# Kernel tuning notes

Hardware: AMD Instinct MI355X
Metric: run time of the kernel (lower is better)

## Reference

```python
import jax, jax.numpy as jnp
import numpy as np

B, S, C, H, E, K = 8, 512, 768, 12, 8, 2
MLP_H = int(C * 4.0)
HD = C // H
ROUTER_REG = 0.01
LN_EPS = 1e-5


def setup_inputs() -> dict:
    key = jax.random.key(0)
    ks = jax.random.split(key, 8)

    def w(k, shape, fan_in):
        return (jax.random.normal(k, shape, dtype=jnp.float32) / np.sqrt(fan_in)).astype(jnp.float32)

    return {
        "x": jax.random.normal(ks[0], (B, S, C), dtype=jnp.float32),
        "expert_tokens": w(ks[1], (E, C), C),
        "ln1_g": jnp.ones((E, C), jnp.float32),
        "ln1_b": jnp.zeros((E, C), jnp.float32),
        "qkv_w": w(ks[2], (E, C, 3 * C), C),
        "qkv_b": jnp.zeros((E, 3 * C), jnp.float32),
        "proj_w": w(ks[3], (E, C, C), C),
        "proj_b": jnp.zeros((E, C), jnp.float32),
        "ln2_g": jnp.ones((E, C), jnp.float32),
        "ln2_b": jnp.zeros((E, C), jnp.float32),
        "fc1_w": w(ks[4], (E, C, MLP_H), C),
        "fc1_b": jnp.zeros((E, MLP_H), jnp.float32),
        "fc2_w": w(ks[5], (E, MLP_H, C), MLP_H),
        "fc2_b": jnp.zeros((E, C), jnp.float32),
    }


def _layernorm(x, g, b):
    mu = jnp.mean(x, axis=-1, keepdims=True)
    var = jnp.mean(jnp.square(x - mu), axis=-1, keepdims=True)
    return (x - mu) * jax.lax.rsqrt(var + LN_EPS) * g + b


def _block(x, p):
    # One transformer Block (pre-LN attention + MLP), params for a single expert.
    ln1_g, ln1_b, qkv_w, qkv_b, proj_w, proj_b, ln2_g, ln2_b, fc1_w, fc1_b, fc2_w, fc2_b = p
    h = _layernorm(x, ln1_g, ln1_b)
    qkv = (h @ qkv_w + qkv_b).reshape(B, S, 3, H, HD)
    q, k, v = qkv[:, :, 0], qkv[:, :, 1], qkv[:, :, 2]  # [B,S,H,HD]
    # NOTE: original code MULTIPLIES by sqrt(head_dim) (scale = head_dim**0.5).
    scale = jnp.float32(np.sqrt(HD))
    attn = jax.nn.softmax(jnp.einsum('bqhd,bkhd->bhqk', q, k) * scale, axis=-1)
    o = jnp.einsum('bhqk,bkhd->bqhd', attn, v).reshape(B, S, C)
    x = x + (o @ proj_w + proj_b)
    h2 = _layernorm(x, ln2_g, ln2_b)
    x = x + (jax.nn.gelu(h2 @ fc1_w + fc1_b, approximate=False) @ fc2_w + fc2_b)
    return x


def reference(x, expert_tokens, ln1_g, ln1_b, qkv_w, qkv_b, proj_w, proj_b,
              ln2_g, ln2_b, fc1_w, fc1_b, fc2_w, fc2_b):
    # Router
    router_logits = jnp.einsum('bsc,nc->bsn', x, expert_tokens) / jnp.float32(np.sqrt(C))
    router_probs = jax.nn.softmax(router_logits, axis=-1)
    top_k_probs, top_k_idx = jax.lax.top_k(router_probs, K)  # [B,S,K]
    top_k_probs = top_k_probs / jnp.sum(top_k_probs, axis=-1, keepdims=True)

    # Dense all-expert compute (sequential over experts to bound memory)
    params = (ln1_g, ln1_b, qkv_w, qkv_b, proj_w, proj_b, ln2_g, ln2_b,
              fc1_w, fc1_b, fc2_w, fc2_b)
    expert_out = jax.lax.map(lambda p: _block(x, p), params)  # [E,B,S,C]
    expert_out = jnp.transpose(expert_out, (1, 2, 0, 3))       # [B,S,E,C]

    # Top-k gather and weighted combine
    sel = jnp.take_along_axis(expert_out, top_k_idx[..., None], axis=2)  # [B,S,K,C]
    combine = jnp.sum(sel * top_k_probs[..., None], axis=2)
    out = x + combine

    # Load-balance auxiliary loss
    counts = jnp.sum(jax.nn.one_hot(top_k_idx, E, dtype=jnp.float32), axis=(0, 1, 2))
    f_i = counts / jnp.float32(B * S * K)
    P_i = jnp.mean(router_probs, axis=(0, 1))
    balance_loss = E * jnp.sum(f_i * P_i) + ROUTER_REG * jnp.linalg.norm(expert_tokens)
    return out, balance_loss
```

## Files before the change

kernel.cpp:

```cpp
#include <hip/hip_runtime.h>
#include <hip/hip_bf16.h>

#define BB 8
#define SS 512
#define CC 768
#define HH 12
#define HD 64
#define EE 8
#define KK 2
#define MLPH 3072
#define NT (BB*SS)
#define NOUT (NT*CC)

#define SLOTB      68059136ull
#define SLOT_U16   34029568ull
#define SLOT_F32   17014784ull

typedef unsigned int u32;
typedef unsigned short u16;
typedef __attribute__((ext_vector_type(8))) short short8;
typedef __attribute__((ext_vector_type(4))) float f32x4;

__device__ __forceinline__ u16 f2bf(float f) {
    u32 u = __builtin_bit_cast(u32, f);
    u32 r = (u + 0x7fffu + ((u >> 16) & 1u)) >> 16;
    return (u16)r;
}
__device__ __forceinline__ float bf2f(u16 h) {
    u32 u = ((u32)h) << 16;
    return __builtin_bit_cast(float, u);
}
__device__ __forceinline__ void gl_lds16(const void* g, void* l) {
    __builtin_amdgcn_global_load_lds(
        (const __attribute__((address_space(1))) u32*)g,
        (__attribute__((address_space(3))) u32*)l, 16, 0, 0);
}
__device__ __forceinline__ void swz_rc(int bid, int& bm, int& bn) {
    int xcd = bid & 7, off = bid >> 3;
    bm = (xcd * 4 + (off & 3)) * 128;
    bn = (off >> 2) * 128;
}

__device__ __forceinline__ void stg_dp(const u16* __restrict__ A, const u16* __restrict__ B,
                                       int ldk, u16* sA, u16* sB, int t, int tid)
{
    int wid = tid >> 6, lane = tid & 63;
#pragma unroll
    for (int rd = 0; rd < 2; rd++) {
        int cb = rd * 256 + wid * 64;
        int c = cb + lane;
        gl_lds16(A + (size_t)(c >> 2) * ldk + t * 32 + (c & 3) * 8, sA + cb * 8);
    }
#pragma unroll
    for (int rd = 0; rd < 2; rd++) {
        int cb = rd * 256 + wid * 64;
        int c = cb + lane;
        gl_lds16(B + (size_t)(c >> 2) * ldk + t * 32 + (c & 3) * 8, sB + cb * 8);
    }
}

__global__ __launch_bounds__(256) void router_kernel(const float* __restrict__ x,
    const float* __restrict__ et, float* __restrict__ W, float* __restrict__ stats)
{
    __shared__ float etl[EE * CC];
    __shared__ float pred[4][2 * EE];
    int tid = threadIdx.x;
    for (int i = tid; i < EE * CC; i += 256) etl[i] = et[i];
    __syncthreads();
    int wid = tid >> 6, lane = tid & 63;
    float psum[EE] = {}, csum[EE] = {};
    for (int i = 0; i < 2; i++) {
        int t = blockIdx.x * 8 + wid * 2 + i;
        const float* xr = x + (size_t)t * CC;
        float acc[EE] = {};
        for (int c = lane; c < CC; c += 64) {
            float xv = xr[c];
#pragma unroll
            for (int e = 0; e < EE; e++) acc[e] += xv * etl[e * CC + c];
        }
#pragma unroll
        for (int e = 0; e < EE; e++)
            for (int off = 1; off < 64; off <<= 1) acc[e] += __shfl_xor(acc[e], off, 64);
        if (lane == 0) {
            const float inv = 0.03608439182435161f;
            float l[EE], m = -1e30f;
#pragma unroll
            for (int e = 0; e < EE; e++) { l[e] = acc[e] * inv; m = fmaxf(m, l[e]); }
            float p[EE], sum = 0.f;
#pragma unroll
            for (int e = 0; e < EE; e++) { p[e] = __expf(l[e] - m); sum += p[e]; }
            int i1 = 0;
#pragma unroll
            for (int e = 1; e < EE; e++) if (p[e] > p[i1]) i1 = e;
            int i2 = -1;
#pragma unroll
            for (int e = 0; e < EE; e++) if (e != i1 && (i2 < 0 || p[e] > p[i2])) i2 = e;
            float wn = p[i1] + p[i2];
#pragma unroll
            for (int e = 0; e < EE; e++) W[t * EE + e] = 0.f;
            W[t * EE + i1] = p[i1] / wn;
            W[t * EE + i2] = p[i2] / wn;
#pragma unroll
            for (int e = 0; e < EE; e++) psum[e] += p[e] / sum;
            csum[i1] += 1.f; csum[i2] += 1.f;
        }
    }
    if (lane == 0) {
#pragma unroll
        for (int e = 0; e < EE; e++) { pred[wid][e] = psum[e]; pred[wid][EE + e] = csum[e]; }
    }
    __syncthreads();
    if (tid < 2 * EE) {
        float s = pred[0][tid] + pred[1][tid] + pred[2][tid] + pred[3][tid];
        atomicAdd(&stats[tid], s);
    }
}

template<int MODE>
__global__ __launch_bounds__(256) void ln_kernel(const float* __restrict__ x, size_t xslot,
    u16* __restrict__ out_hi, u16* __restrict__ out_lo, size_t oslot)
{
    int t = blockIdx.x;
    int eb = blockIdx.y;
    const float* xr = x + (size_t)eb * xslot + (size_t)t * CC;
    __shared__ float red[256];
    int tid = threadIdx.x;
    float v[3];
    float s = 0.f;
#pragma unroll
    for (int i = 0; i < 3; i++) { v[i] = xr[tid + i * 256]; s += v[i]; }
    red[tid] = s; __syncthreads();
    for (int off = 128; off > 0; off >>= 1) { if (tid < off) red[tid] += red[tid + off]; __syncthreads(); }
    float mu = red[0] / (float)CC;
    __syncthreads();
    float s2 = 0.f;
#pragma unroll
    for (int i = 0; i < 3; i++) { float d = v[i] - mu; s2 += d * d; }
    red[tid] = s2; __syncthreads();
    for (int off = 128; off > 0; off >>= 1) { if (tid < off) red[tid] += red[tid + off]; __syncthreads(); }
    float var = red[0] / (float)CC;
    float sc = rsqrtf(var + 1e-5f);
#pragma unroll
    for (int i = 0; i < 3; i++) {
        int c = tid + i * 256;
        float val = (v[i] - mu) * sc;
        u16 hi = f2bf(val);
        out_hi[(size_t)eb * oslot + (size_t)t * CC + c] = hi;
        if (MODE) out_lo[(size_t)eb * oslot + (size_t)t * CC + c] = f2bf(val - bf2f(hi));
    }
}

__global__ __launch_bounds__(256) void prep_expert(
    const float* __restrict__ qkv_w0, const float* __restrict__ qkv_b0,
    const float* __restrict__ proj_w0,
    const float* __restrict__ fc1_w0, const float* __restrict__ fc1_b0,
    const float* __restrict__ fc2_w0,
    const float* __restrict__ g1_0, const float* __restrict__ b1_0,
    const float* __restrict__ g2_0, const float* __restrict__ b2_0,
    u16* __restrict__ qkvTh, u16* __restrict__ qkvTl,
    u16* __restrict__ projT, u16* __restrict__ fc1T, u16* __restrict__ fc2T,
    float* __restrict__ biasq, float* __restrict__ biasf1, int ebase)
{
    __shared__ float tile[32][33];
    __shared__ float bsh[CC];
    __shared__ float redg[256];
    int bid = blockIdx.x;
    int eb = blockIdx.y;
    int ge = ebase + eb;
    int tid = threadIdx.x;
    const float* qkv_w = qkv_w0 + (size_t)ge * CC * 3 * CC;
    const float* qkv_b = qkv_b0 + (size_t)ge * 3 * CC;
    const float* proj_w = proj_w0 + (size_t)ge * CC * CC;
    const float* fc1_w = fc1_w0 + (size_t)ge * CC * MLPH;
    const float* fc1_b = fc1_b0 + (size_t)ge * MLPH;
    const float* fc2_w = fc2_w0 + (size_t)ge * MLPH * CC;
    const float* g1 = g1_0 + (size_t)ge * CC;
    const float* b1 = b1_0 + (size_t)ge * CC;
    const float* g2 = g2_0 + (size_t)ge * CC;
    const float* b2 = b2_0 + (size_t)ge * CC;

    if (bid < 6912) {
        const float* src; const float* scale = nullptr;
        u16 *dh, *dl = nullptr; int N, Kd, n0, k0;
        if (bid < 1728) {
            src = qkv_w; scale = g1;
            dh = qkvTh + (size_t)eb * SLOT_U16; dl = qkvTl + (size_t)eb * SLOT_U16;
            N = 2304; Kd = 768; n0 = (bid % 72) * 32; k0 = (bid / 72) * 32;
        } else if (bid < 2304) {
            int i = bid - 1728;
            src = proj_w; dh = projT + (size_t)eb * SLOT_U16; N = 768; Kd = 768;
            n0 = (i % 24) * 32; k0 = (i / 24) * 32;
        } else if (bid < 4608) {
            int i = bid - 2304;
            src = fc1_w; scale = g2; dh = fc1T + (size_t)eb * SLOT_U16; N = 3072; Kd = 768;
            n0 = (i % 96) * 32; k0 = (i / 96) * 32;
        } else {
            int i = bid - 4608;
            src = fc2_w; dh = fc2T + (size_t)eb * SLOT_U16; N = 768; Kd = 3072;
            n0 = (i % 24) * 32; k0 = (i / 24) * 32;
        }
        int tx = tid & 31, ty = tid >> 5;
#pragma unroll
        for (int i = 0; i < 32; i += 8) {
            float v = src[(size_t)(k0 + ty + i) * N + n0 + tx];
            if (scale) v *= scale[k0 + ty + i];
            tile[ty + i][tx] = v;
        }
        __syncthreads();
#pragma unroll
        for (int i = 0; i < 32; i += 8) {
            float v = tile[tx][ty + i];
            u16 hi = f2bf(v);
            dh[(size_t)(n0 + ty + i) * Kd + k0 + tx] = hi;
            if (dl) dl[(size_t)(n0 + ty + i) * Kd + k0 + tx] = f2bf(v - bf2f(hi));
        }
    } else {
        const float* bv; const float* wsrc; const float* badd;
        float* dst; int N, n0;
        if (bid < 6984) { bv = b1; wsrc = qkv_w; badd = qkv_b; dst = biasq + (size_t)eb * SLOT_F32; N = 2304; n0 = (bid - 6912) * 32; }
        else            { bv = b2; wsrc = fc1_w; badd = fc1_b; dst = biasf1 + (size_t)eb * SLOT_F32; N = MLPH; n0 = (bid - 6984) * 32; }
        for (int i = tid; i < CC; i += 256) bsh[i] = bv[i];
        __syncthreads();
        int g = tid & 31, l8 = tid >> 5;
        int n = n0 + g;
        float acc = 0.f;
        for (int k = l8; k < CC; k += 8) acc += bsh[k] * wsrc[(size_t)k * N + n];
        redg[tid] = acc; __syncthreads();
        if (tid < 32) {
            float sum = 0.f;
#pragma unroll
            for (int i = 0; i < 8; i++) sum += redg[tid + i * 32];
            dst[n0 + tid] = sum + badd[n0 + tid];
        }
    }
}

__global__ __launch_bounds__(256) void gemm_qkv_dp(
    const u16* __restrict__ Ah, const u16* __restrict__ Al,
    const u16* __restrict__ Bh0, const u16* __restrict__ Bl0,
    const float* __restrict__ biasq0, u16* __restrict__ qk_hi0,
    u16* __restrict__ qk_lo0, u16* __restrict__ vtout0)
{
    __shared__ __align__(16) u16 sBh[3][128 * 32];
    __shared__ __align__(16) u16 sBl[3][128 * 32];
    const int NTILE = CC / 32;
    int tid = threadIdx.x;
    int eb = blockIdx.y;
    int bm, bn;
    swz_rc(blockIdx.x, bm, bn);
    bool qk = (bn < 1536);
    int wid = tid >> 6, lane = tid & 63;
    int wr = wid >> 1, wc = wid & 1;
    int la = lane & 15, lb = lane >> 4;

    const u16* Bh = Bh0 + (size_t)eb * SLOT_U16 + (size_t)bn * CC;
    const u16* Bl = Bl0 + (size_t)eb * SLOT_U16 + (size_t)bn * CC;
    const u16* Ahb = Ah + (size_t)bm * CC;
    const u16* Alb = Al + (size_t)bm * CC;

    auto STG = [&](int s, int t) {
#pragma unroll
        for (int rd = 0; rd < 2; rd++) {
            int cb = rd * 256 + wid * 64;
            int c = cb + lane;
            gl_lds16(Bh + (size_t)(c >> 2) * CC + t * 32 + (c & 3) * 8, &sBh[s][(size_t)cb * 8]);
        }
        if (qk) {
#pragma unroll
            for (int rd = 0; rd < 2; rd++) {
                int cb = rd * 256 + wid * 64;
                int c = cb + lane;
                gl_lds16(Bl + (size_t)(c >> 2) * CC + t * 32 + (c & 3) * 8, &sBl[s][(size_t)cb * 8]);
            }
        }
    };

    f32x4 acc[4][4];
#pragma unroll
    for (int i = 0; i < 4; i++)
#pragma unroll
        for (int j = 0; j < 4; j++) acc[i][j] = (f32x4){0.f, 0.f, 0.f, 0.f};

    STG(0, 0);
    STG(1, 1);

    for (int t = 0; t < NTILE; t++) {
        if (t < NTILE - 1) {
            if (qk) asm volatile("s_waitcnt vmcnt(4)" ::: "memory");
            else    asm volatile("s_waitcnt vmcnt(2)" ::: "memory");
        } else {
            asm volatile("s_waitcnt vmcnt(0)" ::: "memory");
        }
        __builtin_amdgcn_s_barrier();
        asm volatile("" ::: "memory");

        short8 avh[4], avl[4];
#pragma unroll
        for (int i = 0; i < 4; i++)
            avh[i] = *(const short8*)(Ahb + (size_t)(wr * 64 + i * 16 + la) * CC + t * 32 + lb * 8);
        if (qk) {
#pragma unroll
            for (int i = 0; i < 4; i++)
                avl[i] = *(const short8*)(Alb + (size_t)(wr * 64 + i * 16 + la) * CC + t * 32 + lb * 8);
        }

        const u16* cBh = &sBh[t % 3][0];
        const u16* cBl = &sBl[t % 3][0];
        __builtin_amdgcn_s_setprio(1);
#pragma unroll
        for (int j = 0; j < 4; j++) {
            short8 bvh = *(const short8*)(cBh + (size_t)(wc * 64 + j * 16 + la) * 32 + lb * 8);
#pragma unroll
            for (int i = 0; i < 4; i++)
                acc[i][j] = __builtin_amdgcn_mfma_f32_16x16x32_bf16(avh[i], bvh, acc[i][j], 0, 0, 0);
        }
        if (qk) {
#pragma unroll
            for (int j = 0; j < 4; j++) {
                short8 bvh = *(const short8*)(cBh + (size_t)(wc * 64 + j * 16 + la) * 32 + lb * 8);
                short8 bvl = *(const short8*)(cBl + (size_t)(wc * 64 + j * 16 + la) * 32 + lb * 8);
#pragma unroll
                for (int i = 0; i < 4; i++) {
                    acc[i][j] = __builtin_amdgcn_mfma_f32_16x16x32_bf16(avh[i], bvl, acc[i][j], 0, 0, 0);
                    acc[i][j] = __builtin_amdgcn_mfma_f32_16x16x32_bf16(avl[i], bvh, acc[i][j], 0, 0, 0);
                }
            }
        }
        __builtin_amdgcn_s_setprio(0);

        if (t + 2 < NTILE) STG((t + 2) % 3, t + 2);
    }

    const float* bias = biasq0 + (size_t)eb * SLOT_F32;
    u16* qk_hi = qk_hi0 + (size_t)eb * SLOT_U16;
    u16* qk_lo = qk_lo0 + (size_t)eb * SLOT_U16;
    u16* vtout = vtout0 + (size_t)eb * SLOT_U16;
#pragma unroll
    for (int i = 0; i < 4; i++) {
#pragma unroll
        for (int j = 0; j < 4; j++) {
            int gn = bn + wc * 64 + j * 16 + la;
            float bsv = bias[gn];
#pragma unroll
            for (int r = 0; r < 4; r++) {
                int gm = bm + wr * 64 + i * 16 + lb * 4 + r;
                float v = acc[i][j][r] + bsv;
                if (gn < 1536) {
                    u16 hi = f2bf(v);
                    qk_hi[(size_t)gm * 1536 + gn] = hi;
                    qk_lo[(size_t)gm * 1536 + gn] = f2bf(v - bf2f(hi));
                } else {
                    int dd = (gn - 1536) & 63, hh = (gn - 1536) >> 6;
                    int ss = gm & (SS - 1), bb = gm >> 9;
                    vtout[((size_t)((bb * HH + hh) * HD + dd)) * SS + ss] = f2bf(v);
                }
            }
        }
    }
}

template<int EPI>
__device__ __forceinline__ void gemm_dp_body(
    const u16* __restrict__ Ab, const u16* __restrict__ Bb, int Kdim,
    const float* __restrict__ biasp, const float* __restrict__ resp,
    const float* __restrict__ Wt, int ge, const float* __restrict__ xinit,
    void* __restrict__ Cout, int N, int bm, int bn)
{
    __shared__ __align__(16) u16 sA[3][128 * 32];
    __shared__ __align__(16) u16 sB[3][128 * 32];
    int tid = threadIdx.x;
    int wid = tid >> 6, lane = tid & 63;
    int wr = wid >> 1, wc = wid & 1;
    int la = lane & 15, lb = lane >> 4;
    int NTILE = Kdim / 32;

    f32x4 acc[4][4];
#pragma unroll
    for (int i = 0; i < 4; i++)
#pragma unroll
        for (int j = 0; j < 4; j++) acc[i][j] = (f32x4){0.f, 0.f, 0.f, 0.f};

    stg_dp(Ab, Bb, Kdim, sA[0], sB[0], 0, tid);
    stg_dp(Ab, Bb, Kdim, sA[1], sB[1], 1, tid);

    for (int t = 0; t < NTILE; t++) {
        if (t < NTILE - 1) asm volatile("s_waitcnt vmcnt(4)" ::: "memory");
        else               asm volatile("s_waitcnt vmcnt(0)" ::: "memory");
        __builtin_amdgcn_s_barrier();
        asm volatile("" ::: "memory");

        const u16* cA = &sA[t % 3][0];
        const u16* cB = &sB[t % 3][0];
        __builtin_amdgcn_s_setprio(1);
        short8 bv[4];
#pragma unroll
        for (int j = 0; j < 4; j++)
            bv[j] = *(const short8*)(cB + ((size_t)(wc * 64 + j * 16 + la) * 4 + lb) * 8);
#pragma unroll
        for (int i = 0; i < 4; i++) {
            short8 av = *(const short8*)(cA + ((size_t)(wr * 64 + i * 16 + la) * 4 + lb) * 8);
#pragma unroll
            for (int j = 0; j < 4; j++)
                acc[i][j] = __builtin_amdgcn_mfma_f32_16x16x32_bf16(av, bv[j], acc[i][j], 0, 0, 0);
        }
        __builtin_amdgcn_s_setprio(0);

        if (t + 2 < NTILE) stg_dp(Ab, Bb, Kdim, sA[(t + 2) % 3], sB[(t + 2) % 3], t + 2, tid);
    }

#pragma unroll
    for (int i = 0; i < 4; i++) {
#pragma unroll
        for (int j = 0; j < 4; j++) {
            int gn = bn + wc * 64 + j * 16 + la;
            float bsv = biasp[gn];
#pragma unroll
            for (int r = 0; r < 4; r++) {
                int gm = bm + wr * 64 + i * 16 + lb * 4 + r;
                size_t idx = (size_t)gm * N + gn;
                float v = acc[i][j][r] + bsv;
                if (EPI == 1) {
                    ((float*)Cout)[idx] = resp[idx] + v;
                } else if (EPI == 2) {
                    float gel = 0.5f * v * (1.0f + erff(v * 0.70710678118654752f));
                    ((u16*)Cout)[idx] = f2bf(gel);
                } else {
                    float w = Wt[(size_t)gm * EE + ge];
                    float val = w * (v + resp[idx]);
                    if (ge == 0) val += xinit[idx];
                    atomicAdd(&((float*)Cout)[idx], val);
                }
            }
        }
    }
}

__global__ __launch_bounds__(256) void gemm_proj_dp(
    const u16* __restrict__ A0, const u16* __restrict__ BT0,
    const float* __restrict__ bias0, const float* __restrict__ x,
    float* __restrict__ C0)
{
    int eb = blockIdx.y;
    int bm, bn;
    swz_rc(blockIdx.x, bm, bn);
    gemm_dp_body<1>(A0 + (size_t)eb * SLOT_U16 + (size_t)bm * CC,
                    BT0 + (size_t)eb * SLOT_U16 + (size_t)bn * CC, CC,
                    bias0 + (size_t)eb * CC, x, nullptr, 0, nullptr,
                    C0 + (size_t)eb * SLOT_F32, CC, bm, bn);
}

__global__ __launch_bounds__(256) void gemm_fc1_dp(
    const u16* __restrict__ A0, const u16* __restrict__ BT0,
    const float* __restrict__ bias0, u16* __restrict__ C0)
{
    int eb = blockIdx.y;
    int bm, bn;
    swz_rc(blockIdx.x, bm, bn);
    gemm_dp_body<2>(A0 + (size_t)eb * SLOT_U16 + (size_t)bm * CC,
                    BT0 + (size_t)eb * SLOT_U16 + (size_t)bn * CC, CC,
                    bias0 + (size_t)eb * SLOT_F32, nullptr, nullptr, 0, nullptr,
                    C0 + (size_t)eb * SLOT_U16, MLPH, bm, bn);
}

__global__ __launch_bounds__(256) void gemm_fc2_dp(
    const u16* __restrict__ A0, const u16* __restrict__ BT0,
    const float* __restrict__ bias0, const float* __restrict__ res0,
    const float* __restrict__ Wt, int ebase, const float* __restrict__ xinit,
    float* __restrict__ Cout)
{
    int eb = blockIdx.y;
    int bm, bn;
    swz_rc(blockIdx.x, bm, bn);
    gemm_dp_body<5>(A0 + (size_t)eb * SLOT_U16 + (size_t)bm * MLPH,
                    BT0 + (size_t)eb * SLOT_U16 + (size_t)bn * MLPH, MLPH,
                    bias0 + (size_t)eb * CC, res0 + (size_t)eb * SLOT_F32,
                    Wt, ebase + eb, xinit, Cout, CC, bm, bn);
}

__global__ __launch_bounds__(256) void attn_mfma(const u16* __restrict__ qk_hi0,
    const u16* __restrict__ qk_lo0, const u16* __restrict__ vt0, u16* __restrict__ o0)
{
    int q0 = blockIdx.x * 64;
    int h = blockIdx.y;
    int z = blockIdx.z;
    int b = z & (BB - 1), eb = z >> 3;
    int tid = threadIdx.x, wid = tid >> 6, lane = tid & 63;
    int la = lane & 15, lb = lane >> 4;
    __shared__ __align__(16) u16 Ksh[64 * 64];
    __shared__ __align__(16) u16 Ksl[64 * 64];
    __shared__ __align__(16) u16 Vs[64 * 64];
    __shared__ __align__(16) u16 Ps[4][16 * 64];

    const u16* qk_hi = qk_hi0 + (size_t)eb * SLOT_U16;
    const u16* qk_lo = qk_lo0 + (size_t)eb * SLOT_U16;
    const u16* vt = vt0 + (size_t)eb * SLOT_U16;
    u16* o = o0 + (size_t)eb * SLOT_U16;

    short8 aqh[2], aql[2];
    {
        size_t qoff = (size_t)(b * SS + q0 + wid * 16 + la) * 1536 + h * HD;
#pragma unroll
        for (int kc = 0; kc < 2; kc++) {
            aqh[kc] = *(const short8*)(qk_hi + qoff + kc * 32 + lb * 8);
            aql[kc] = *(const short8*)(qk_lo + qoff + kc * 32 + lb * 8);
        }
    }
    const u16* kbh = qk_hi + (size_t)(b * SS) * 1536 + CC + h * HD;
    const u16* kbl = qk_lo + (size_t)(b * SS) * 1536 + CC + h * HD;
    const u16* vtbase = vt + (size_t)((b * HH + h) * HD) * SS;

    float m_r[4], l_r[4];
    f32x4 acc_o[4];
#pragma unroll
    for (int r = 0; r < 4; r++) { m_r[r] = -1e30f; l_r[r] = 0.f; }
#pragma unroll
    for (int d0 = 0; d0 < 4; d0++) acc_o[d0] = (f32x4){0.f, 0.f, 0.f, 0.f};

    for (int kt = 0; kt < SS; kt += 64) {
#pragma unroll
        for (int it = 0; it < 2; it++) {
            int base = it * 256 + wid * 64;
            int c = base + lane;
            int row = c >> 3;
            int gk = (c & 7) ^ (row & 7);
            gl_lds16(kbh + (size_t)(kt + row) * 1536 + gk * 8, Ksh + base * 8);
            gl_lds16(kbl + (size_t)(kt + row) * 1536 + gk * 8, Ksl + base * 8);
            gl_lds16(vtbase + (size_t)row * SS + kt + gk * 8, Vs + base * 8);
        }
        __syncthreads();

        f32x4 s4[4];
#pragma unroll
        for (int j = 0; j < 4; j++) s4[j] = (f32x4){0.f, 0.f, 0.f, 0.f};
#pragma unroll
        for (int kc = 0; kc < 2; kc++)
#pragma unroll
            for (int j = 0; j < 4; j++) {
                size_t off = (size_t)(j * 16 + la) * 64 + (((kc * 4 + lb) ^ (la & 7)) * 8);
                short8 bkh = *(const short8*)(Ksh + off);
                short8 bkl = *(const short8*)(Ksl + off);
                s4[j] = __builtin_amdgcn_mfma_f32_16x16x32_bf16(aqh[kc], bkh, s4[j], 0, 0, 0);
                s4[j] = __builtin_amdgcn_mfma_f32_16x16x32_bf16(aql[kc], bkh, s4[j], 0, 0, 0);
                s4[j] = __builtin_amdgcn_mfma_f32_16x16x32_bf16(aqh[kc], bkl, s4[j], 0, 0, 0);
            }
#pragma unroll
        for (int j = 0; j < 4; j++) s4[j] = s4[j] * 8.f;

#pragma unroll
        for (int r = 0; r < 4; r++) {
            float mx = fmaxf(fmaxf(s4[0][r], s4[1][r]), fmaxf(s4[2][r], s4[3][r]));
#pragma unroll
            for (int off = 1; off < 16; off <<= 1) mx = fmaxf(mx, __shfl_xor(mx, off, 64));
            float mn = fmaxf(m_r[r], mx);
            float corr = __expf(m_r[r] - mn);
            m_r[r] = mn;
            float rs = 0.f;
#pragma unroll
            for (int j = 0; j < 4; j++) {
                float p = __expf(s4[j][r] - mn);
                s4[j][r] = p; rs += p;
            }
#pragma unroll
            for (int off = 1; off < 16; off <<= 1) rs += __shfl_xor(rs, off, 64);
            l_r[r] = l_r[r] * corr + rs;
#pragma unroll
            for (int d0 = 0; d0 < 4; d0++) acc_o[d0][r] = acc_o[d0][r] * corr;
        }
#pragma unroll
        for (int j = 0; j < 4; j++)
#pragma unroll
            for (int r = 0; r < 4; r++) {
                int row = lb * 4 + r;
                int sg = (2 * j + (la >> 3)) ^ (row & 7);
                Ps[wid][row * 64 + sg * 8 + (la & 7)] = f2bf(s4[j][r]);
            }
        short8 pa[2];
#pragma unroll
        for (int kc = 0; kc < 2; kc++)
            pa[kc] = *(const short8*)(&Ps[wid][la * 64 + (((kc * 4 + lb) ^ (la & 7)) * 8)]);
#pragma unroll
        for (int d0 = 0; d0 < 4; d0++)
#pragma unroll
            for (int kc = 0; kc < 2; kc++) {
                short8 bv = *(const short8*)(&Vs[(d0 * 16 + la) * 64 + (((kc * 4 + lb) ^ (la & 7)) * 8)]);
                acc_o[d0] = __builtin_amdgcn_mfma_f32_16x16x32_bf16(pa[kc], bv, acc_o[d0], 0, 0, 0);
            }
        __syncthreads();
    }
#pragma unroll
    for (int r = 0; r < 4; r++) {
        float invl = 1.f / l_r[r];
        int tok = b * SS + q0 + wid * 16 + lb * 4 + r;
#pragma unroll
        for (int d0 = 0; d0 < 4; d0++)
            o[(size_t)tok * CC + h * HD + d0 * 16 + la] = f2bf(acc_o[d0][r] * invl);
    }
}

__global__ __launch_bounds__(256) void loss_kernel(const float* __restrict__ et,
    const float* __restrict__ stats, float* __restrict__ out_loss)
{
    __shared__ float red[256];
    int tid = threadIdx.x;
    float s = 0.f;
    for (int i = tid; i < EE * CC; i += 256) { float v = et[i]; s += v * v; }
    red[tid] = s; __syncthreads();
    for (int off = 128; off > 0; off >>= 1) { if (tid < off) red[tid] += red[tid + off]; __syncthreads(); }
    if (tid == 0) {
        float bl = 0.f;
        for (int e = 0; e < EE; e++) {
            float f = stats[EE + e] / (float)(NT * KK);
            float P = stats[e] / (float)NT;
            bl += f * P;
        }
        *out_loss = (float)EE * bl + 0.01f * sqrtf(red[0]);
    }
}

extern "C" void kernel_launch(void* const* d_in, const int* in_sizes, int n_in,
                              void* d_out, int out_size, void* d_ws, size_t ws_size,
                              hipStream_t stream) {
    const float* x      = (const float*)d_in[0];
    const float* et     = (const float*)d_in[1];
    const float* ln1_g  = (const float*)d_in[2];
    const float* ln1_b  = (const float*)d_in[3];
    const float* qkv_w  = (const float*)d_in[4];
    const float* qkv_b  = (const float*)d_in[5];
    const float* proj_w = (const float*)d_in[6];
    const float* proj_b = (const float*)d_in[7];
    const float* ln2_g  = (const float*)d_in[8];
    const float* ln2_b  = (const float*)d_in[9];
    const float* fc1_w  = (const float*)d_in[10];
    const float* fc1_b  = (const float*)d_in[11];
    const float* fc2_w  = (const float*)d_in[12];
    const float* fc2_b  = (const float*)d_in[13];
    float* outp = (float*)d_out;
    char* base = (char*)d_ws;

    const size_t FIXED = 12714496;
    int EB = 1;
    if (ws_size >= FIXED + 8 * SLOTB) EB = 8;
    else if (ws_size >= FIXED + 4 * SLOTB) EB = 4;
    else if (ws_size >= FIXED + 2 * SLOTB) EB = 2;

    float* W      = (float*)(base);
    float* stats  = (float*)(base + 131072);
    u16*   xh_hi  = (u16*)  (base + 131584);
    u16*   xh_lo  = (u16*)  (base + 6423040);
    char* slot0 = base + FIXED;
    u16*   qkvTh  = (u16*)  (slot0);
    u16*   qkvTl  = (u16*)  (slot0 + 3538944);
    u16*   projT  = (u16*)  (slot0 + 7077888);
    u16*   fc1T   = (u16*)  (slot0 + 8257536);
    u16*   fc2T   = (u16*)  (slot0 + 12976128);
    float* biasq  = (float*)(slot0 + 17694720);
    float* biasf1 = (float*)(slot0 + 17711104);
    u16*   qk_hi  = (u16*)  (slot0 + 17727488);
    u16*   qk_lo  = (u16*)  (slot0 + 30310400);
    u16*   mlp1   = (u16*)  (slot0 + 17727488);
    u16*   vtb    = (u16*)  (slot0 + 42893312);
    u16*   xmhat  = (u16*)  (slot0 + 42893312);
    u16*   obf    = (u16*)  (slot0 + 49184768);
    float* xmid   = (float*)(slot0 + 55476224);

    hipMemsetAsync(stats, 0, 16 * sizeof(float), stream);
    hipMemsetAsync(outp, 0, (size_t)NOUT * sizeof(float), stream);

    router_kernel<<<NT / 8, 256, 0, stream>>>(x, et, W, stats);
    ln_kernel<1><<<dim3(NT, 1), 256, 0, stream>>>(x, 0, xh_hi, xh_lo, 0);

    for (int ebase = 0; ebase < EE; ebase += EB) {
        prep_expert<<<dim3(7080, EB), 256, 0, stream>>>(
            qkv_w, qkv_b, proj_w, fc1_w, fc1_b, fc2_w,
            ln1_g, ln1_b, ln2_g, ln2_b,
            qkvTh, qkvTl, projT, fc1T, fc2T, biasq, biasf1, ebase);

        gemm_qkv_dp<<<dim3(18 * 32, EB), 256, 0, stream>>>(
            xh_hi, xh_lo, qkvTh, qkvTl, biasq, qk_hi, qk_lo, vtb);

        attn_mfma<<<dim3(SS / 64, HH, BB * EB), 256, 0, stream>>>(qk_hi, qk_lo, vtb, obf);

        gemm_proj_dp<<<dim3(6 * 32, EB), 256, 0, stream>>>(
            obf, projT, proj_b + (size_t)ebase * CC, x, xmid);

        ln_kernel<0><<<dim3(NT, EB), 256, 0, stream>>>(xmid, SLOT_F32, xmhat, nullptr, SLOT_U16);

        gemm_fc1_dp<<<dim3(24 * 32, EB), 256, 0, stream>>>(xmhat, fc1T, biasf1, mlp1);

        gemm_fc2_dp<<<dim3(6 * 32, EB), 256, 0, stream>>>(
            mlp1, fc2T, fc2_b + (size_t)ebase * CC, xmid, W, ebase, x, outp);
    }

    loss_kernel<<<1, 256, 0, stream>>>(et, stats, outp + NOUT);
}
```

Baseline: 1.595 ms.

## Split QKV GEMM into uniform Q/K split-bf16 and V GEMMs with transpose

Splits the fused QKV GEMM, which branched per block between 3-pass split-bf16 for Q/K and single-pass for V, into two kernels. The Q/K kernel now runs the three hi/lo products as a flat 72-step K loop, staging both A and B tiles into LDS instead of reading A fragments straight from global memory. V goes through the generic pipelined GEMM body with a plain bf16 store. A separate transpose kernel then builds the V^T layout that attention expects, replacing the scattered transposed stores. This removes divergent block work and uncoalesced writes, at the cost of two extra launches and an extra round-trip of V through memory.

```diff
diff --git a/kernel.cpp b/kernel.cpp
--- a/kernel.cpp
+++ b/kernel.cpp
@@ -41,21 +41,21 @@
     bn = (off >> 2) * 128;
 }
 
-__device__ __forceinline__ void stg_dp(const u16* __restrict__ A, const u16* __restrict__ B,
-                                       int ldk, u16* sA, u16* sB, int t, int tid)
+__device__ __forceinline__ void stg_dp2(const u16* __restrict__ A, const u16* __restrict__ B,
+                                        int ldk, int koff, u16* sA, u16* sB, int tid)
 {
     int wid = tid >> 6, lane = tid & 63;
 #pragma unroll
     for (int rd = 0; rd < 2; rd++) {
         int cb = rd * 256 + wid * 64;
         int c = cb + lane;
-        gl_lds16(A + (size_t)(c >> 2) * ldk + t * 32 + (c & 3) * 8, sA + cb * 8);
+        gl_lds16(A + (size_t)(c >> 2) * ldk + koff + (c & 3) * 8, sA + cb * 8);
     }
 #pragma unroll
     for (int rd = 0; rd < 2; rd++) {
         int cb = rd * 256 + wid * 64;
         int c = cb + lane;
-        gl_lds16(B + (size_t)(c >> 2) * ldk + t * 32 + (c & 3) * 8, sB + cb * 8);
+        gl_lds16(B + (size_t)(c >> 2) * ldk + koff + (c & 3) * 8, sB + cb * 8);
     }
 }
 
@@ -235,44 +235,33 @@
     }
 }
 
-__global__ __launch_bounds__(256) void gemm_qkv_dp(
+__global__ __launch_bounds__(256) void gemm_qk_dp(
     const u16* __restrict__ Ah, const u16* __restrict__ Al,
     const u16* __restrict__ Bh0, const u16* __restrict__ Bl0,
     const float* __restrict__ biasq0, u16* __restrict__ qk_hi0,
-    u16* __restrict__ qk_lo0, u16* __restrict__ vtout0)
-{
-    __shared__ __align__(16) u16 sBh[3][128 * 32];
-    __shared__ __align__(16) u16 sBl[3][128 * 32];
-    const int NTILE = CC / 32;
+    u16* __restrict__ qk_lo0)
+{
+    __shared__ __align__(16) u16 sA[3][128 * 32];
+    __shared__ __align__(16) u16 sB[3][128 * 32];
+    const int NTILE = 72;
     int tid = threadIdx.x;
     int eb = blockIdx.y;
     int bm, bn;
     swz_rc(blockIdx.x, bm, bn);
-    bool qk = (bn < 1536);
     int wid = tid >> 6, lane = tid & 63;
     int wr = wid >> 1, wc = wid & 1;
     int la = lane & 15, lb = lane >> 4;
 
-    const u16* Bh = Bh0 + (size_t)eb * SLOT_U16 + (size_t)bn * CC;
-    const u16* Bl = Bl0 + (size_t)eb * SLOT_U16 + (size_t)bn * CC;
     const u16* Ahb = Ah + (size_t)bm * CC;
     const u16* Alb = Al + (size_t)bm * CC;
+    const u16* Bhb = Bh0 + (size_t)eb * SLOT_U16 + (size_t)bn * CC;
+    const u16* Blb = Bl0 + (size_t)eb * SLOT_U16 + (size_t)bn * CC;
 
     auto STG = [&](int s, int t) {
-#pragma unroll
-        for (int rd = 0; rd < 2; rd++) {
-            int cb = rd * 256 + wid * 64;
-            int c = cb + lane;
-            gl_lds16(Bh + (size_t)(c >> 2) * CC + t * 32 + (c & 3) * 8, &sBh[s][(size_t)cb * 8]);
-        }
-        if (qk) {
-#pragma unroll
-            for (int rd = 0; rd < 2; rd++) {
-                int cb = rd * 256 + wid * 64;
-                int c = cb + lane;
-                gl_lds16(Bl + (size_t)(c >> 2) * CC + t * 32 + (c & 3) * 8, &sBl[s][(size_t)cb * 8]);
-            }
-        }
+        int tt = (t < 24) ? t : (t < 48 ? t - 24 : t - 48);
+        const u16* Ap = (t < 48) ? Ahb : Alb;
+        const u16* Bp = (t < 24) ? Bhb : (t < 48 ? Blb : Bhb);
+        stg_dp2(Ap, Bp, CC, tt * 32, sA[s], sB[s], tid);
     };
 
     f32x4 acc[4][4];
@@ -285,46 +274,24 @@
     STG(1, 1);
 
     for (int t = 0; t < NTILE; t++) {
-        if (t < NTILE - 1) {
-            if (qk) asm volatile("s_waitcnt vmcnt(4)" ::: "memory");
-            else    asm volatile("s_waitcnt vmcnt(2)" ::: "memory");
-        } else {
-            asm volatile("s_waitcnt vmcnt(0)" ::: "memory");
-        }
+        if (t < NTILE - 1) asm volatile("s_waitcnt vmcnt(4)" ::: "memory");
+        else               asm volatile("s_waitcnt vmcnt(0)" ::: "memory");
         __builtin_amdgcn_s_barrier();
         asm volatile("" ::: "memory");
 
-        short8 avh[4], avl[4];
-#pragma unroll
-        for (int i = 0; i < 4; i++)
-            avh[i] = *(const short8*)(Ahb + (size_t)(wr * 64 + i * 16 + la) * CC + t * 32 + lb * 8);
-        if (qk) {
-#pragma unroll
-            for (int i = 0; i < 4; i++)
-                avl[i] = *(const short8*)(Alb + (size_t)(wr * 64 + i * 16 + la) * CC + t * 32 + lb * 8);
-        }
-
-        const u16* cBh = &sBh[t % 3][0];
-        const u16* cBl = &sBl[t % 3][0];
+        const u16* cA = &sA[t % 3][0];
+        const u16* cB = &sB[t % 3][0];
         __builtin_amdgcn_s_setprio(1);
-#pragma unroll
-        for (int j = 0; j < 4; j++) {
-            short8 bvh = *(const short8*)(cBh + (size_t)(wc * 64 + j * 16 + la) * 32 + lb * 8);
-#pragma unroll
-            for (int i = 0; i < 4; i++)
-                acc[i][j] = __builtin_amdgcn_mfma_f32_16x16x32_bf16(avh[i], bvh, acc[i][j], 0, 0, 0);
-        }
-        if (qk) {
-#pragma unroll
-            for (int j = 0; j < 4; j++) {
-                short8 bvh = *(const short8*)(cBh + (size_t)(wc * 64 + j * 16 + la) * 32 + lb * 8);
-                short8 bvl = *(const short8*)(cBl + (size_t)(wc * 64 + j * 16 + la) * 32 + lb * 8);
-#pragma unroll
-                for (int i = 0; i < 4; i++) {
-                    acc[i][j] = __builtin_amdgcn_mfma_f32_16x16x32_bf16(avh[i], bvl, acc[i][j], 0, 0, 0);
-                    acc[i][j] = __builtin_amdgcn_mfma_f32_16x16x32_bf16(avl[i], bvh, acc[i][j], 0, 0, 0);
-                }
-            }
+        short8 bv[4];
+#pragma unroll
+        for (int j = 0; j < 4; j++)
+            bv[j] = *(const short8*)(cB + ((size_t)(wc * 64 + j * 16 + la) * 4 + lb) * 8);
+#pragma unroll
+        for (int i = 0; i < 4; i++) {
+            short8 av = *(const short8*)(cA + ((size_t)(wr * 64 + i * 16 + la) * 4 + lb) * 8);
+#pragma unroll
+            for (int j = 0; j < 4; j++)
+                acc[i][j] = __builtin_amdgcn_mfma_f32_16x16x32_bf16(av, bv[j], acc[i][j], 0, 0, 0);
         }
         __builtin_amdgcn_s_setprio(0);
 
@@ -334,7 +301,6 @@
     const float* bias = biasq0 + (size_t)eb * SLOT_F32;
     u16* qk_hi = qk_hi0 + (size_t)eb * SLOT_U16;
     u16* qk_lo = qk_lo0 + (size_t)eb * SLOT_U16;
-    u16* vtout = vtout0 + (size_t)eb * SLOT_U16;
 #pragma unroll
     for (int i = 0; i < 4; i++) {
 #pragma unroll
@@ -345,15 +311,9 @@
             for (int r = 0; r < 4; r++) {
                 int gm = bm + wr * 64 + i * 16 + lb * 4 + r;
                 float v = acc[i][j][r] + bsv;
-                if (gn < 1536) {
-                    u16 hi = f2bf(v);
-                    qk_hi[(size_t)gm * 1536 + gn] = hi;
-                    qk_lo[(size_t)gm * 1536 + gn] = f2bf(v - bf2f(hi));
-                } else {
-                    int dd = (gn - 1536) & 63, hh = (gn - 1536) >> 6;
-                    int ss = gm & (SS - 1), bb = gm >> 9;
-                    vtout[((size_t)((bb * HH + hh) * HD + dd)) * SS + ss] = f2bf(v);
-                }
+                u16 hi = f2bf(v);
+                qk_hi[(size_t)gm * 1536 + gn] = hi;
+                qk_lo[(size_t)gm * 1536 + gn] = f2bf(v - bf2f(hi));
             }
         }
     }
@@ -380,8 +340,8 @@
 #pragma unroll
         for (int j = 0; j < 4; j++) acc[i][j] = (f32x4){0.f, 0.f, 0.f, 0.f};
 
-    stg_dp(Ab, Bb, Kdim, sA[0], sB[0], 0, tid);
-    stg_dp(Ab, Bb, Kdim, sA[1], sB[1], 1, tid);
+    stg_dp2(Ab, Bb, Kdim, 0, sA[0], sB[0], tid);
+    stg_dp2(Ab, Bb, Kdim, 32, sA[1], sB[1], tid);
 
     for (int t = 0; t < NTILE; t++) {
         if (t < NTILE - 1) asm volatile("s_waitcnt vmcnt(4)" ::: "memory");
@@ -405,7 +365,7 @@
         }
         __builtin_amdgcn_s_setprio(0);
 
-        if (t + 2 < NTILE) stg_dp(Ab, Bb, Kdim, sA[(t + 2) % 3], sB[(t + 2) % 3], t + 2, tid);
+        if (t + 2 < NTILE) stg_dp2(Ab, Bb, Kdim, (t + 2) * 32, sA[(t + 2) % 3], sB[(t + 2) % 3], tid);
     }
 
 #pragma unroll
@@ -424,6 +384,8 @@
                 } else if (EPI == 2) {
                     float gel = 0.5f * v * (1.0f + erff(v * 0.70710678118654752f));
                     ((u16*)Cout)[idx] = f2bf(gel);
+                } else if (EPI == 7) {
+                    ((u16*)Cout)[idx] = f2bf(v);
                 } else {
                     float w = Wt[(size_t)gm * EE + ge];
                     float val = w * (v + resp[idx]);
@@ -435,6 +397,19 @@
     }
 }
 
+__global__ __launch_bounds__(256) void gemm_v_dp(
+    const u16* __restrict__ A0, const u16* __restrict__ BT0,
+    const float* __restrict__ biasq0, u16* __restrict__ C0)
+{
+    int eb = blockIdx.y;
+    int bm, bn;
+    swz_rc(blockIdx.x, bm, bn);
+    gemm_dp_body<7>(A0 + (size_t)bm * CC,
+                    BT0 + (size_t)eb * SLOT_U16 + (size_t)(1536 + bn) * CC, CC,
+                    biasq0 + (size_t)eb * SLOT_F32 + 1536, nullptr, nullptr, 0, nullptr,
+                    C0 + (size_t)eb * SLOT_U16, CC, bm, bn);
+}
+
 __global__ __launch_bounds__(256) void gemm_proj_dp(
     const u16* __restrict__ A0, const u16* __restrict__ BT0,
     const float* __restrict__ bias0, const float* __restrict__ x,
@@ -475,6 +450,38 @@
                     BT0 + (size_t)eb * SLOT_U16 + (size_t)bn * MLPH, MLPH,
                     bias0 + (size_t)eb * CC, res0 + (size_t)eb * SLOT_F32,
                     Wt, ebase + eb, xinit, Cout, CC, bm, bn);
+}
+
+__global__ __launch_bounds__(256) void vtrans(const u16* __restrict__ vraw0,
+    u16* __restrict__ vt0)
+{
+    __shared__ u16 tile[64][65];
+    int st = blockIdx.x;
+    int h = blockIdx.y;
+    int z = blockIdx.z;
+    int b = z & (BB - 1), eb = z >> 3;
+    const u16* vraw = vraw0 + (size_t)eb * SLOT_U16;
+    u16* vt = vt0 + (size_t)eb * SLOT_U16;
+    int tid = threadIdx.x;
+    int row = tid >> 3, ch = tid & 7;
+#pragma unroll
+    for (int it = 0; it < 2; it++) {
+        int s = it * 32 + row;
+        const u16* src = vraw + (size_t)(b * SS + st * 64 + s) * CC + h * HD + ch * 8;
+        short8 v = *(const short8*)src;
+#pragma unroll
+        for (int k = 0; k < 8; k++) tile[s][ch * 8 + k] = (u16)v[k];
+    }
+    __syncthreads();
+#pragma unroll
+    for (int it = 0; it < 2; it++) {
+        int d = it * 32 + row;
+        u16* dst = vt + ((size_t)((b * HH + h) * HD + d)) * SS + st * 64 + ch * 8;
+        short8 v;
+#pragma unroll
+        for (int k = 0; k < 8; k++) v[k] = (short)tile[ch * 8 + k][d];
+        *(short8*)dst = v;
+    }
 }
 
 __global__ __launch_bounds__(256) void attn_mfma(const u16* __restrict__ qk_hi0,
@@ -661,6 +668,7 @@
     u16*   vtb    = (u16*)  (slot0 + 42893312);
     u16*   xmhat  = (u16*)  (slot0 + 42893312);
     u16*   obf    = (u16*)  (slot0 + 49184768);
+    u16*   vraw   = obf;
     float* xmid   = (float*)(slot0 + 55476224);
 
     hipMemsetAsync(stats, 0, 16 * sizeof(float), stream);
@@ -675,8 +683,12 @@
             ln1_g, ln1_b, ln2_g, ln2_b,
             qkvTh, qkvTl, projT, fc1T, fc2T, biasq, biasf1, ebase);
 
-        gemm_qkv_dp<<<dim3(18 * 32, EB), 256, 0, stream>>>(
-            xh_hi, xh_lo, qkvTh, qkvTl, biasq, qk_hi, qk_lo, vtb);
+        gemm_qk_dp<<<dim3(12 * 32, EB), 256, 0, stream>>>(
+            xh_hi, xh_lo, qkvTh, qkvTl, biasq, qk_hi, qk_lo);
+
+        gemm_v_dp<<<dim3(6 * 32, EB), 256, 0, stream>>>(xh_hi, qkvTh, biasq, vraw);
+
+        vtrans<<<dim3(SS / 64, HH, BB * EB), 256, 0, stream>>>(vraw, vtb);
 
         attn_mfma<<<dim3(SS / 64, HH, BB * EB), 256, 0, stream>>>(qk_hi, qk_lo, vtb, obf);
 
```

Result: no change. 1.598 ms (+0.2%).
